# Kernel tuning notes

Hardware: AMD Instinct MI355X
Metric: run time of the kernel (lower is better)

## Reference

```python
import jax, jax.numpy as jnp
import numpy as np

N_NODES = 100000
N_EDGES = 1600000
IN_F = 128
HID = 16
NEG_SLOPE = 0.2


def setup_inputs() -> dict:
    key = jax.random.key(0)
    ks = jax.random.split(key, 12)
    x = jax.random.normal(ks[0], (N_NODES, IN_F), dtype=jnp.float32)
    edge_index = jax.random.randint(ks[1], (2, N_EDGES), 0, N_NODES, dtype=jnp.int32)
    s1 = 1.0 / np.sqrt(IN_F)
    s2 = 1.0 / np.sqrt(2 * HID)
    # layer 1: heads=2, out=16, concat -> 32
    W1 = jax.random.normal(ks[2], (IN_F, 2 * HID), dtype=jnp.float32) * s1
    a_src1 = jax.random.normal(ks[3], (2, HID), dtype=jnp.float32) * s2
    a_dst1 = jax.random.normal(ks[4], (2, HID), dtype=jnp.float32) * s2
    b1 = jnp.zeros((2 * HID,), dtype=jnp.float32)
    # layer 2: heads=1, out=1
    W2 = jax.random.normal(ks[5], (2 * HID, 1), dtype=jnp.float32) * s2
    a_src2 = jax.random.normal(ks[6], (1, 1), dtype=jnp.float32)
    a_dst2 = jax.random.normal(ks[7], (1, 1), dtype=jnp.float32)
    b2 = jnp.zeros((1,), dtype=jnp.float32)
    return {"x": x, "edge_index": edge_index, "W1": W1, "a_src1": a_src1,
            "a_dst1": a_dst1, "b1": b1, "W2": W2, "a_src2": a_src2,
            "a_dst2": a_dst2, "b2": b2}


def gat_conv(x, src, dst, W, a_src, a_dst, bias, heads, out_ch, concat):
    # PyG GATConv: linear proj, per-edge leaky-relu score, segment softmax over
    # incoming edges (dst), scatter-add aggregation. Self loops already in src/dst.
    n = x.shape[0]
    h = (x @ W).reshape(n, heads, out_ch)                      # [N,H,C]
    alpha_s = (h * a_src[None]).sum(-1)                        # [N,H]
    alpha_d = (h * a_dst[None]).sum(-1)                        # [N,H]
    e = jax.nn.leaky_relu(alpha_s[src] + alpha_d[dst], NEG_SLOPE)  # [E,H]
    m = jax.lax.stop_gradient(jax.ops.segment_max(e, dst, num_segments=n))
    ex = jnp.exp(e - m[dst])
    denom = jax.ops.segment_sum(ex, dst, num_segments=n)       # [N,H]
    alpha = ex / (denom[dst] + 1e-16)                          # [E,H]
    out = jax.ops.segment_sum(alpha[..., None] * h[src], dst, num_segments=n)  # [N,H,C]
    out = out.reshape(n, heads * out_ch) if concat else out.mean(axis=1)
    return out + bias


def reference(x, edge_index, W1, a_src1, a_dst1, b1, W2, a_src2, a_dst2, b2):
    n = x.shape[0]
    loop = jnp.arange(n, dtype=edge_index.dtype)
    src = jnp.concatenate([edge_index[0], loop])
    dst = jnp.concatenate([edge_index[1], loop])
    h = jax.nn.elu(gat_conv(x, src, dst, W1, a_src1, a_dst1, b1, 2, HID, True))
    out = gat_conv(h, src, dst, W2, a_src2, a_dst2, b2, 1, 1, False)
    return out
```

## Files before the change

kernel.cpp:

```cpp
#include <hip/hip_runtime.h>
#include <math.h>

#define IN_F 128
#define C1 32
#define NEG 0.2f
#define XPAD 132
#define BSZ 256
#define CAP 4992
#define EPB 2048

typedef _Float16 h16;
typedef _Float16 h16x2 __attribute__((ext_vector_type(2)));
typedef _Float16 h16x4 __attribute__((ext_vector_type(4)));

__device__ __forceinline__ float leaky(float x) { return x >= 0.f ? x : NEG * x; }

__global__ __launch_bounds__(256)
void k_fat(const float* __restrict__ x, const float* __restrict__ W1,
           const float* __restrict__ a_s, const float* __restrict__ a_d,
           h16* __restrict__ h1h, float* __restrict__ as1,
           float* __restrict__ ad1, int N,
           const int* __restrict__ ei, int E, int ET, int nbk,
           int* __restrict__ bcnt, int* __restrict__ ebuf, int nproj) {
    __shared__ float smem[IN_F * C1 + 32 * XPAD];
    int t = threadIdx.x;
    if ((int)blockIdx.x < nproj) {
        float* Wl = smem;
        float(*xs)[XPAD] = (float(*)[XPAD])(smem + IN_F * C1);
        for (int i = t; i < IN_F * C1 / 4; i += 256)
            ((float4*)Wl)[i] = ((const float4*)W1)[i];
        int nl = t >> 3, colq = t & 7;
        int node = blockIdx.x * 32 + nl;
        if (node < N) {
            const float4* xr = (const float4*)(x + (size_t)node * IN_F);
            #pragma unroll
            for (int q = 0; q < 4; ++q) {
                int f4 = colq + q * 8;
                *(float4*)&xs[nl][f4 * 4] = xr[f4];
            }
        }
        __syncthreads();
        if (node >= N) return;
        float4 acc = {0.f, 0.f, 0.f, 0.f};
        const float4* wp = (const float4*)Wl;
        #pragma unroll 4
        for (int k4 = 0; k4 < IN_F / 4; ++k4) {
            float4 xv = *(const float4*)&xs[nl][k4 * 4];
            float4 w0 = wp[(k4 * 4 + 0) * 8 + colq];
            float4 w1 = wp[(k4 * 4 + 1) * 8 + colq];
            float4 w2 = wp[(k4 * 4 + 2) * 8 + colq];
            float4 w3 = wp[(k4 * 4 + 3) * 8 + colq];
            acc.x = fmaf(xv.x, w0.x, acc.x); acc.y = fmaf(xv.x, w0.y, acc.y);
            acc.z = fmaf(xv.x, w0.z, acc.z); acc.w = fmaf(xv.x, w0.w, acc.w);
            acc.x = fmaf(xv.y, w1.x, acc.x); acc.y = fmaf(xv.y, w1.y, acc.y);
            acc.z = fmaf(xv.y, w1.z, acc.z); acc.w = fmaf(xv.y, w1.w, acc.w);
            acc.x = fmaf(xv.z, w2.x, acc.x); acc.y = fmaf(xv.z, w2.y, acc.y);
            acc.z = fmaf(xv.z, w2.z, acc.z); acc.w = fmaf(xv.z, w2.w, acc.w);
            acc.x = fmaf(xv.w, w3.x, acc.x); acc.y = fmaf(xv.w, w3.y, acc.y);
            acc.z = fmaf(xv.w, w3.z, acc.z); acc.w = fmaf(xv.w, w3.w, acc.w);
        }
        h16x4 hv = { (h16)acc.x, (h16)acc.y, (h16)acc.z, (h16)acc.w };
        *(h16x4*)(h1h + (size_t)node * C1 + colq * 4) = hv;
        int cb = colq * 4;
        float sv = acc.x * a_s[cb] + acc.y * a_s[cb + 1] + acc.z * a_s[cb + 2] + acc.w * a_s[cb + 3];
        float dv = acc.x * a_d[cb] + acc.y * a_d[cb + 1] + acc.z * a_d[cb + 2] + acc.w * a_d[cb + 3];
        sv += __shfl_xor(sv, 1); dv += __shfl_xor(dv, 1);
        sv += __shfl_xor(sv, 2); dv += __shfl_xor(dv, 2);
        if (colq == 0) { as1[node * 2 + 0] = sv; ad1[node * 2 + 0] = dv; }
        if (colq == 4) { as1[node * 2 + 1] = sv; ad1[node * 2 + 1] = dv; }
    } else {
        int* hist = (int*)smem;
        int* lcur = hist + 512;
        int2* ecache = (int2*)(lcur + 512);
        int bid = blockIdx.x - nproj;
        hist[t] = 0; hist[t + 256] = 0;
        __syncthreads();
        int i0 = bid * EPB, i1 = min(ET, i0 + EPB);
        for (int i = i0 + t; i < i1; i += 256) {
            int s, d;
            if (i < E) { s = ei[i]; d = ei[E + i]; } else { s = d = i - E; }
            ecache[i - i0] = make_int2(s, d);
            atomicAdd(&hist[d >> 8], 1);
        }
        __syncthreads();
        for (int b = t; b < nbk; b += 256) {
            int h = hist[b];
            int base = h ? atomicAdd(&bcnt[b], h) : 0;
            lcur[b] = b * CAP + base;
        }
        __syncthreads();
        for (int i = i0 + t; i < i1; i += 256) {
            int2 e = ecache[i - i0];
            int bkt = e.y >> 8;
            int pos = atomicAdd(&lcur[bkt], 1);
            if (pos < (bkt + 1) * CAP)
                ebuf[pos] = (e.x << 8) | (e.y & 255);
        }
    }
}

__global__ __launch_bounds__(256)
void k_bcsr(const int* __restrict__ bcnt, const int* __restrict__ ebuf,
            int N, int nbk, int ET,
            const float* __restrict__ as1, const float* __restrict__ ad1,
            int* __restrict__ off, int2* __restrict__ csr2) {
    __shared__ int deg[256];
    __shared__ int cur[256];
    __shared__ float adl[512];
    __shared__ int red[4];
    int b = blockIdx.x, t = threadIdx.x;
    int part = 0;
    for (int k = t; k < b; k += 256) part += min(bcnt[k], CAP);
    part += __shfl_xor(part, 1);  part += __shfl_xor(part, 2);
    part += __shfl_xor(part, 4);  part += __shfl_xor(part, 8);
    part += __shfl_xor(part, 16); part += __shfl_xor(part, 32);
    if ((t & 63) == 0) red[t >> 6] = part;
    int cnt = min(bcnt[b], CAP);
    int ebase = b * CAP;
    int n0 = b * BSZ;
    deg[t] = 0;
    if (n0 + t < N) ((float2*)adl)[t] = ((const float2*)ad1)[n0 + t];
    __syncthreads();
    int fbase = red[0] + red[1] + red[2] + red[3];
    if (b == nbk - 1 && t == 0) off[N] = fbase + cnt;
    for (int i = t; i < cnt; i += 256)
        atomicAdd(&deg[ebuf[ebase + i] & 255], 1);
    __syncthreads();
    int v = deg[t];
    __syncthreads();
    for (int o = 1; o < 256; o <<= 1) {
        int xv = (t >= o) ? deg[t - o] : 0; __syncthreads();
        deg[t] += xv; __syncthreads();
    }
    int excl = deg[t] - v;
    if (n0 + t < N) off[n0 + t] = fbase + excl;
    cur[t] = fbase + excl;
    __syncthreads();
    for (int i = t; i < cnt; i += 256) {
        int e = ebuf[ebase + i];
        int dl = e & 255;
        int s = e >> 8;
        float2 asv = ((const float2*)as1)[s];
        float w0 = __expf(leaky(asv.x + adl[dl * 2 + 0]));
        float w1 = __expf(leaky(asv.y + adl[dl * 2 + 1]));
        h16x2 wp = { (h16)w0, (h16)w1 };
        int p = atomicAdd(&cur[dl], 1);
        int2 rec; rec.x = s; rec.y = *(int*)&wp;
        csr2[p] = rec;
    }
}

__global__ __launch_bounds__(256)
void k_l1agg(const int* __restrict__ off, const int2* __restrict__ csr2,
             const h16* __restrict__ h1h, const float* __restrict__ b1,
             const float* __restrict__ W2, float* __restrict__ p2, int N) {
    int t = threadIdx.x;
    int node = blockIdx.x * 32 + (t >> 3);
    if (node >= N) return;
    int l = t & 7;
    int c0 = l * 4;
    int head = l >> 2;
    float den = 0.f, a0 = 0.f, a1 = 0.f, a2 = 0.f, a3 = 0.f;
    int j0 = off[node], j1 = off[node + 1];
    for (int j = j0; j < j1; j += 4) {
        #pragma unroll
        for (int k = 0; k < 4; ++k) {
            int jj = j + k;
            bool valid = jj < j1;
            jj = valid ? jj : j0;
            int2 e = csr2[jj];
            int s = e.x;
            h16x2 wv = *(h16x2*)&e.y;
            float w = valid ? (float)(head ? wv.y : wv.x) : 0.f;
            h16x4 hv = *(const h16x4*)(h1h + ((size_t)s << 5) + c0);
            den += w;
            a0 = fmaf(w, (float)hv.x, a0);
            a1 = fmaf(w, (float)hv.y, a1);
            a2 = fmaf(w, (float)hv.z, a2);
            a3 = fmaf(w, (float)hv.w, a3);
        }
    }
    float inv = 1.f / (den + 1e-16f);
    float o, val = 0.f;
    o = a0 * inv + b1[c0 + 0]; o = o > 0.f ? o : expm1f(o); val = fmaf(o, W2[c0 + 0], val);
    o = a1 * inv + b1[c0 + 1]; o = o > 0.f ? o : expm1f(o); val = fmaf(o, W2[c0 + 1], val);
    o = a2 * inv + b1[c0 + 2]; o = o > 0.f ? o : expm1f(o); val = fmaf(o, W2[c0 + 2], val);
    o = a3 * inv + b1[c0 + 3]; o = o > 0.f ? o : expm1f(o); val = fmaf(o, W2[c0 + 3], val);
    val += __shfl_xor(val, 1); val += __shfl_xor(val, 2); val += __shfl_xor(val, 4);
    if (l == 0) p2[node] = val;
}

__global__ void k_l2(const int* __restrict__ off, const int2* __restrict__ csr2,
                     const float* __restrict__ p2, const float* __restrict__ as2,
                     const float* __restrict__ ad2, const float* __restrict__ b2,
                     float* __restrict__ out, int N) {
    int i = blockIdx.x * blockDim.x + threadIdx.x;
    if (i >= N) return;
    float A = as2[0];
    float Bc = ad2[0] * p2[i];
    float den = 0.f, num = 0.f;
    int j0 = off[i], j1 = off[i + 1];
    for (int j = j0; j < j1; j += 4) {
        #pragma unroll
        for (int k = 0; k < 4; ++k) {
            int jj = j + k;
            bool valid = jj < j1;
            int s = csr2[valid ? jj : j0].x;
            float ps = p2[s];
            float w = valid ? __expf(leaky(fmaf(ps, A, Bc))) : 0.f;
            den += w;
            num = fmaf(w, ps, num);
        }
    }
    out[i] = num / (den + 1e-16f) + b2[0];
}

extern "C" void kernel_launch(void* const* d_in, const int* in_sizes, int n_in,
                              void* d_out, int out_size, void* d_ws, size_t ws_size,
                              hipStream_t stream) {
    const float* x    = (const float*)d_in[0];
    const int*   ei   = (const int*)d_in[1];
    const float* W1   = (const float*)d_in[2];
    const float* a_s1 = (const float*)d_in[3];
    const float* a_d1 = (const float*)d_in[4];
    const float* b1   = (const float*)d_in[5];
    const float* W2   = (const float*)d_in[6];
    const float* a_s2 = (const float*)d_in[7];
    const float* a_d2 = (const float*)d_in[8];
    const float* b2   = (const float*)d_in[9];
    float* out = (float*)d_out;

    const int N  = in_sizes[0] / IN_F;
    const int E  = in_sizes[1] / 2;
    const int ET = E + N;
    const int nbk = (N + BSZ - 1) / BSZ;

    float* w   = (float*)d_ws;
    float* as1 = w; w += (size_t)2 * N;
    float* ad1 = w; w += (size_t)2 * N;
    float* p2  = w; w += (size_t)N;
    h16* h1h   = (h16*)w;
    w += (size_t)16 * N;
    int* iw     = (int*)w;
    int* bcnt   = iw; iw += 512;
    int* off    = iw; iw += (N + 1);
    iw += (iw - (int*)d_ws) & 1;
    int2* csr2  = (int2*)iw; iw += (size_t)2 * ET;
    int* ebuf   = iw; iw += (size_t)nbk * CAP;

    const int B = 256;
    const int nproj = (N + 31) / 32;
    const int nblkA = (ET + EPB - 1) / EPB;

    hipMemsetAsync(bcnt, 0, 512 * sizeof(int), stream);
    k_fat  <<<nproj + nblkA, B, 0, stream>>>(x, W1, a_s1, a_d1, h1h, as1, ad1, N,
                                             ei, E, ET, nbk, bcnt, ebuf, nproj);
    k_bcsr <<<nbk, B, 0, stream>>>(bcnt, ebuf, N, nbk, ET, as1, ad1, off, csr2);
    k_l1agg<<<(N + 31) / 32, B, 0, stream>>>(off, csr2, h1h, b1, W2, p2, N);
    k_l2   <<<(N + B - 1) / B, B, 0, stream>>>(off, csr2, p2, a_s2, a_d2, b2, out, N);
}
```

Baseline: 211.8 us.

## Compute 128 nodes per projection block, batch edge loads, split layer-2 across lanes

The projection path now handles four nodes per thread group, 128 nodes per block. It reads x straight from global memory instead of staging it in shared memory, so each W1 value loaded from LDS is reused across four rows and LDS use shrinks. The CSR fill loop issues four ebuf/as1 gathers before using any of them, to expose more memory-level parallelism. Layer-2 aggregation now splits each node's edges over four lanes with shuffle reductions, which improves load balance. The trade-off is uncoalesced direct x reads, since each lane reads a different row, and possible register pressure.

```diff
diff --git a/kernel.cpp b/kernel.cpp
--- a/kernel.cpp
+++ b/kernel.cpp
@@ -4,7 +4,6 @@
 #define IN_F 128
 #define C1 32
 #define NEG 0.2f
-#define XPAD 132
 #define BSZ 256
 #define CAP 4992
 #define EPB 2048
@@ -22,54 +21,65 @@
            float* __restrict__ ad1, int N,
            const int* __restrict__ ei, int E, int ET, int nbk,
            int* __restrict__ bcnt, int* __restrict__ ebuf, int nproj) {
-    __shared__ float smem[IN_F * C1 + 32 * XPAD];
+    __shared__ int smem[5120];
     int t = threadIdx.x;
     if ((int)blockIdx.x < nproj) {
-        float* Wl = smem;
-        float(*xs)[XPAD] = (float(*)[XPAD])(smem + IN_F * C1);
+        float* Wl = (float*)smem;
         for (int i = t; i < IN_F * C1 / 4; i += 256)
             ((float4*)Wl)[i] = ((const float4*)W1)[i];
-        int nl = t >> 3, colq = t & 7;
-        int node = blockIdx.x * 32 + nl;
-        if (node < N) {
-            const float4* xr = (const float4*)(x + (size_t)node * IN_F);
-            #pragma unroll
-            for (int q = 0; q < 4; ++q) {
-                int f4 = colq + q * 8;
-                *(float4*)&xs[nl][f4 * 4] = xr[f4];
-            }
-        }
-        __syncthreads();
-        if (node >= N) return;
-        float4 acc = {0.f, 0.f, 0.f, 0.f};
+        __syncthreads();
+        int colq = t & 7, g = t >> 3;
+        int base = blockIdx.x * 128;
         const float4* wp = (const float4*)Wl;
-        #pragma unroll 4
+        int nn[4]; const float4* xp[4];
+        #pragma unroll
+        for (int j = 0; j < 4; ++j) {
+            int node = base + g + 32 * j;
+            nn[j] = node;
+            int cl = node < N ? node : 0;
+            xp[j] = (const float4*)(x + (size_t)cl * IN_F);
+        }
+        float4 acc[4];
+        #pragma unroll
+        for (int j = 0; j < 4; ++j) acc[j] = make_float4(0.f, 0.f, 0.f, 0.f);
+        #pragma unroll 2
         for (int k4 = 0; k4 < IN_F / 4; ++k4) {
-            float4 xv = *(const float4*)&xs[nl][k4 * 4];
             float4 w0 = wp[(k4 * 4 + 0) * 8 + colq];
             float4 w1 = wp[(k4 * 4 + 1) * 8 + colq];
             float4 w2 = wp[(k4 * 4 + 2) * 8 + colq];
             float4 w3 = wp[(k4 * 4 + 3) * 8 + colq];
-            acc.x = fmaf(xv.x, w0.x, acc.x); acc.y = fmaf(xv.x, w0.y, acc.y);
-            acc.z = fmaf(xv.x, w0.z, acc.z); acc.w = fmaf(xv.x, w0.w, acc.w);
-            acc.x = fmaf(xv.y, w1.x, acc.x); acc.y = fmaf(xv.y, w1.y, acc.y);
-            acc.z = fmaf(xv.y, w1.z, acc.z); acc.w = fmaf(xv.y, w1.w, acc.w);
-            acc.x = fmaf(xv.z, w2.x, acc.x); acc.y = fmaf(xv.z, w2.y, acc.y);
-            acc.z = fmaf(xv.z, w2.z, acc.z); acc.w = fmaf(xv.z, w2.w, acc.w);
-            acc.x = fmaf(xv.w, w3.x, acc.x); acc.y = fmaf(xv.w, w3.y, acc.y);
-            acc.z = fmaf(xv.w, w3.z, acc.z); acc.w = fmaf(xv.w, w3.w, acc.w);
-        }
-        h16x4 hv = { (h16)acc.x, (h16)acc.y, (h16)acc.z, (h16)acc.w };
-        *(h16x4*)(h1h + (size_t)node * C1 + colq * 4) = hv;
+            #pragma unroll
+            for (int j = 0; j < 4; ++j) {
+                float4 xv = xp[j][k4];
+                acc[j].x = fmaf(xv.x, w0.x, acc[j].x); acc[j].y = fmaf(xv.x, w0.y, acc[j].y);
+                acc[j].z = fmaf(xv.x, w0.z, acc[j].z); acc[j].w = fmaf(xv.x, w0.w, acc[j].w);
+                acc[j].x = fmaf(xv.y, w1.x, acc[j].x); acc[j].y = fmaf(xv.y, w1.y, acc[j].y);
+                acc[j].z = fmaf(xv.y, w1.z, acc[j].z); acc[j].w = fmaf(xv.y, w1.w, acc[j].w);
+                acc[j].x = fmaf(xv.z, w2.x, acc[j].x); acc[j].y = fmaf(xv.z, w2.y, acc[j].y);
+                acc[j].z = fmaf(xv.z, w2.z, acc[j].z); acc[j].w = fmaf(xv.z, w2.w, acc[j].w);
+                acc[j].x = fmaf(xv.w, w3.x, acc[j].x); acc[j].y = fmaf(xv.w, w3.y, acc[j].y);
+                acc[j].z = fmaf(xv.w, w3.z, acc[j].z); acc[j].w = fmaf(xv.w, w3.w, acc[j].w);
+            }
+        }
         int cb = colq * 4;
-        float sv = acc.x * a_s[cb] + acc.y * a_s[cb + 1] + acc.z * a_s[cb + 2] + acc.w * a_s[cb + 3];
-        float dv = acc.x * a_d[cb] + acc.y * a_d[cb + 1] + acc.z * a_d[cb + 2] + acc.w * a_d[cb + 3];
-        sv += __shfl_xor(sv, 1); dv += __shfl_xor(dv, 1);
-        sv += __shfl_xor(sv, 2); dv += __shfl_xor(dv, 2);
-        if (colq == 0) { as1[node * 2 + 0] = sv; ad1[node * 2 + 0] = dv; }
-        if (colq == 4) { as1[node * 2 + 1] = sv; ad1[node * 2 + 1] = dv; }
+        float as0 = a_s[cb], as1c = a_s[cb + 1], as2c = a_s[cb + 2], as3 = a_s[cb + 3];
+        float ad0 = a_d[cb], ad1c = a_d[cb + 1], ad2c = a_d[cb + 2], ad3 = a_d[cb + 3];
+        #pragma unroll
+        for (int j = 0; j < 4; ++j) {
+            bool vld = nn[j] < N;
+            if (vld) {
+                h16x4 hv = { (h16)acc[j].x, (h16)acc[j].y, (h16)acc[j].z, (h16)acc[j].w };
+                *(h16x4*)(h1h + (size_t)nn[j] * C1 + cb) = hv;
+            }
+            float sv = acc[j].x * as0 + acc[j].y * as1c + acc[j].z * as2c + acc[j].w * as3;
+            float dv = acc[j].x * ad0 + acc[j].y * ad1c + acc[j].z * ad2c + acc[j].w * ad3;
+            sv += __shfl_xor(sv, 1); dv += __shfl_xor(dv, 1);
+            sv += __shfl_xor(sv, 2); dv += __shfl_xor(dv, 2);
+            if (vld && colq == 0) { as1[nn[j] * 2 + 0] = sv; ad1[nn[j] * 2 + 0] = dv; }
+            if (vld && colq == 4) { as1[nn[j] * 2 + 1] = sv; ad1[nn[j] * 2 + 1] = dv; }
+        }
     } else {
-        int* hist = (int*)smem;
+        int* hist = smem;
         int* lcur = hist + 512;
         int2* ecache = (int2*)(lcur + 512);
         int bid = blockIdx.x - nproj;
@@ -136,17 +146,28 @@
     if (n0 + t < N) off[n0 + t] = fbase + excl;
     cur[t] = fbase + excl;
     __syncthreads();
-    for (int i = t; i < cnt; i += 256) {
-        int e = ebuf[ebase + i];
-        int dl = e & 255;
-        int s = e >> 8;
-        float2 asv = ((const float2*)as1)[s];
-        float w0 = __expf(leaky(asv.x + adl[dl * 2 + 0]));
-        float w1 = __expf(leaky(asv.y + adl[dl * 2 + 1]));
-        h16x2 wp = { (h16)w0, (h16)w1 };
-        int p = atomicAdd(&cur[dl], 1);
-        int2 rec; rec.x = s; rec.y = *(int*)&wp;
-        csr2[p] = rec;
+    const float2* as1v = (const float2*)as1;
+    for (int i = t; i < cnt; i += 1024) {
+        int e4[4]; float2 a4[4];
+        #pragma unroll
+        for (int k = 0; k < 4; ++k) {
+            int idx = i + k * 256;
+            bool vd = idx < cnt;
+            int e = ebuf[ebase + (vd ? idx : 0)];
+            e4[k] = vd ? e : -1;
+            a4[k] = as1v[e >> 8];
+        }
+        #pragma unroll
+        for (int k = 0; k < 4; ++k) {
+            if (e4[k] < 0) continue;
+            int dl = e4[k] & 255, s = e4[k] >> 8;
+            float w0 = __expf(leaky(a4[k].x + adl[dl * 2 + 0]));
+            float w1 = __expf(leaky(a4[k].y + adl[dl * 2 + 1]));
+            h16x2 wpk = { (h16)w0, (h16)w1 };
+            int p = atomicAdd(&cur[dl], 1);
+            int2 rec; rec.x = s; rec.y = *(int*)&wpk;
+            csr2[p] = rec;
+        }
     }
 }
 
@@ -190,29 +211,33 @@
     if (l == 0) p2[node] = val;
 }
 
-__global__ void k_l2(const int* __restrict__ off, const int2* __restrict__ csr2,
-                     const float* __restrict__ p2, const float* __restrict__ as2,
-                     const float* __restrict__ ad2, const float* __restrict__ b2,
-                     float* __restrict__ out, int N) {
-    int i = blockIdx.x * blockDim.x + threadIdx.x;
-    if (i >= N) return;
+__global__ __launch_bounds__(256)
+void k_l2(const int* __restrict__ off, const int2* __restrict__ csr2,
+          const float* __restrict__ p2, const float* __restrict__ as2,
+          const float* __restrict__ ad2, const float* __restrict__ b2,
+          float* __restrict__ out, int N) {
+    int t = threadIdx.x;
+    int node = blockIdx.x * 64 + (t >> 2);
+    if (node >= N) return;
+    int l = t & 3;
     float A = as2[0];
-    float Bc = ad2[0] * p2[i];
+    float Bc = ad2[0] * p2[node];
     float den = 0.f, num = 0.f;
-    int j0 = off[i], j1 = off[i + 1];
-    for (int j = j0; j < j1; j += 4) {
-        #pragma unroll
-        for (int k = 0; k < 4; ++k) {
-            int jj = j + k;
-            bool valid = jj < j1;
-            int s = csr2[valid ? jj : j0].x;
-            float ps = p2[s];
-            float w = valid ? __expf(leaky(fmaf(ps, A, Bc))) : 0.f;
-            den += w;
-            num = fmaf(w, ps, num);
-        }
-    }
-    out[i] = num / (den + 1e-16f) + b2[0];
+    int j0 = off[node], j1 = off[node + 1];
+    for (int j = j0 + l; j < j1; j += 8) {
+        int s0 = csr2[j].x;
+        int jb = j + 4;
+        bool vb = jb < j1;
+        int s1 = csr2[vb ? jb : j].x;
+        float ps0 = p2[s0], ps1 = p2[s1];
+        float w0 = __expf(leaky(fmaf(ps0, A, Bc)));
+        float w1 = vb ? __expf(leaky(fmaf(ps1, A, Bc))) : 0.f;
+        den += w0 + w1;
+        num = fmaf(w0, ps0, fmaf(w1, ps1, num));
+    }
+    den += __shfl_xor(den, 1); den += __shfl_xor(den, 2);
+    num += __shfl_xor(num, 1); num += __shfl_xor(num, 2);
+    if (l == 0) out[node] = num / (den + 1e-16f) + b2[0];
 }
 
 extern "C" void kernel_launch(void* const* d_in, const int* in_sizes, int n_in,
@@ -249,7 +274,7 @@
     int* ebuf   = iw; iw += (size_t)nbk * CAP;
 
     const int B = 256;
-    const int nproj = (N + 31) / 32;
+    const int nproj = (N + 127) / 128;
     const int nblkA = (ET + EPB - 1) / EPB;
 
     hipMemsetAsync(bcnt, 0, 512 * sizeof(int), stream);
@@ -257,5 +282,5 @@
                                              ei, E, ET, nbk, bcnt, ebuf, nproj);
     k_bcsr <<<nbk, B, 0, stream>>>(bcnt, ebuf, N, nbk, ET, as1, ad1, off, csr2);
     k_l1agg<<<(N + 31) / 32, B, 0, stream>>>(off, csr2, h1h, b1, W2, p2, N);
-    k_l2   <<<(N + B - 1) / B, B, 0, stream>>>(off, csr2, p2, a_s2, a_d2, b2, out, N);
-}
+    k_l2   <<<(N + 63) / 64, B, 0, stream>>>(off, csr2, p2, a_s2, a_d2, b2, out, N);
+}
```

Result: slower. 221.4 us (+4.5%).

## Aggregate both GAT layers directly from destination buckets with shared-memory atomics

Applied to the files above, without the earlier changes.

Removes the CSR build kernel and the per-node offset array. Both layers now aggregate straight from the bucketed edge buffer, one block per 128-node bucket, accumulating numerators and denominators in LDS with float atomics. Bucket size halves to 128 nodes, so the histogram and cursor arrays in the edge-binning path grow. The aim is to cut the extra global pass that wrote and reread the CSR records. The cost is heavy LDS atomic traffic, fewer and larger blocks, and edge order that is no longer deterministic.

```diff
diff --git a/kernel.cpp b/kernel.cpp
--- a/kernel.cpp
+++ b/kernel.cpp
@@ -5,12 +5,11 @@
 #define C1 32
 #define NEG 0.2f
 #define XPAD 132
-#define BSZ 256
-#define CAP 4992
+#define BSZ 128
+#define CAP 2560
 #define EPB 2048
 
 typedef _Float16 h16;
-typedef _Float16 h16x2 __attribute__((ext_vector_type(2)));
 typedef _Float16 h16x4 __attribute__((ext_vector_type(4)));
 
 __device__ __forceinline__ float leaky(float x) { return x >= 0.f ? x : NEG * x; }
@@ -70,17 +69,17 @@
         if (colq == 4) { as1[node * 2 + 1] = sv; ad1[node * 2 + 1] = dv; }
     } else {
         int* hist = (int*)smem;
-        int* lcur = hist + 512;
-        int2* ecache = (int2*)(lcur + 512);
+        int* lcur = hist + 1024;
+        int2* ecache = (int2*)(lcur + 1024);
         int bid = blockIdx.x - nproj;
-        hist[t] = 0; hist[t + 256] = 0;
+        hist[t] = 0; hist[t + 256] = 0; hist[t + 512] = 0; hist[t + 768] = 0;
         __syncthreads();
         int i0 = bid * EPB, i1 = min(ET, i0 + EPB);
         for (int i = i0 + t; i < i1; i += 256) {
             int s, d;
             if (i < E) { s = ei[i]; d = ei[E + i]; } else { s = d = i - E; }
             ecache[i - i0] = make_int2(s, d);
-            atomicAdd(&hist[d >> 8], 1);
+            atomicAdd(&hist[d >> 7], 1);
         }
         __syncthreads();
         for (int b = t; b < nbk; b += 256) {
@@ -91,128 +90,95 @@
         __syncthreads();
         for (int i = i0 + t; i < i1; i += 256) {
             int2 e = ecache[i - i0];
-            int bkt = e.y >> 8;
+            int bkt = e.y >> 7;
             int pos = atomicAdd(&lcur[bkt], 1);
             if (pos < (bkt + 1) * CAP)
-                ebuf[pos] = (e.x << 8) | (e.y & 255);
-        }
-    }
-}
-
-__global__ __launch_bounds__(256)
-void k_bcsr(const int* __restrict__ bcnt, const int* __restrict__ ebuf,
-            int N, int nbk, int ET,
-            const float* __restrict__ as1, const float* __restrict__ ad1,
-            int* __restrict__ off, int2* __restrict__ csr2) {
-    __shared__ int deg[256];
-    __shared__ int cur[256];
-    __shared__ float adl[512];
-    __shared__ int red[4];
+                ebuf[pos] = (e.x << 7) | (e.y & 127);
+        }
+    }
+}
+
+__global__ __launch_bounds__(512)
+void k_agg1(const int* __restrict__ bcnt, const int* __restrict__ ebuf,
+            int N, const float* __restrict__ as1, const float* __restrict__ ad1,
+            const float* __restrict__ b1, const float* __restrict__ W2,
+            const h16* __restrict__ h1h, float* __restrict__ p2) {
+    __shared__ float acc[BSZ][33];
+    __shared__ float den[BSZ * 3];
+    __shared__ float adl[BSZ * 2];
     int b = blockIdx.x, t = threadIdx.x;
-    int part = 0;
-    for (int k = t; k < b; k += 256) part += min(bcnt[k], CAP);
-    part += __shfl_xor(part, 1);  part += __shfl_xor(part, 2);
-    part += __shfl_xor(part, 4);  part += __shfl_xor(part, 8);
-    part += __shfl_xor(part, 16); part += __shfl_xor(part, 32);
-    if ((t & 63) == 0) red[t >> 6] = part;
     int cnt = min(bcnt[b], CAP);
     int ebase = b * CAP;
-    int n0 = b * BSZ;
-    deg[t] = 0;
-    if (n0 + t < N) ((float2*)adl)[t] = ((const float2*)ad1)[n0 + t];
-    __syncthreads();
-    int fbase = red[0] + red[1] + red[2] + red[3];
-    if (b == nbk - 1 && t == 0) off[N] = fbase + cnt;
-    for (int i = t; i < cnt; i += 256)
-        atomicAdd(&deg[ebuf[ebase + i] & 255], 1);
-    __syncthreads();
-    int v = deg[t];
-    __syncthreads();
-    for (int o = 1; o < 256; o <<= 1) {
-        int xv = (t >= o) ? deg[t - o] : 0; __syncthreads();
-        deg[t] += xv; __syncthreads();
-    }
-    int excl = deg[t] - v;
-    if (n0 + t < N) off[n0 + t] = fbase + excl;
-    cur[t] = fbase + excl;
-    __syncthreads();
-    for (int i = t; i < cnt; i += 256) {
+    int n0 = b << 7;
+    for (int i = t; i < BSZ * 33; i += 512) ((float*)acc)[i] = 0.f;
+    for (int i = t; i < BSZ * 3; i += 512) den[i] = 0.f;
+    if (t < BSZ) {
+        int n = n0 + t;
+        float2 v = (n < N) ? ((const float2*)ad1)[n] : make_float2(0.f, 0.f);
+        adl[t * 2] = v.x; adl[t * 2 + 1] = v.y;
+    }
+    __syncthreads();
+    int slot = t >> 3, l = t & 7, c0 = l * 4;
+    for (int i = slot; i < cnt; i += 64) {
         int e = ebuf[ebase + i];
-        int dl = e & 255;
-        int s = e >> 8;
+        int dl = e & 127, s = e >> 7;
         float2 asv = ((const float2*)as1)[s];
         float w0 = __expf(leaky(asv.x + adl[dl * 2 + 0]));
         float w1 = __expf(leaky(asv.y + adl[dl * 2 + 1]));
-        h16x2 wp = { (h16)w0, (h16)w1 };
-        int p = atomicAdd(&cur[dl], 1);
-        int2 rec; rec.x = s; rec.y = *(int*)&wp;
-        csr2[p] = rec;
-    }
-}
-
-__global__ __launch_bounds__(256)
-void k_l1agg(const int* __restrict__ off, const int2* __restrict__ csr2,
-             const h16* __restrict__ h1h, const float* __restrict__ b1,
-             const float* __restrict__ W2, float* __restrict__ p2, int N) {
-    int t = threadIdx.x;
-    int node = blockIdx.x * 32 + (t >> 3);
-    if (node >= N) return;
-    int l = t & 7;
-    int c0 = l * 4;
-    int head = l >> 2;
-    float den = 0.f, a0 = 0.f, a1 = 0.f, a2 = 0.f, a3 = 0.f;
-    int j0 = off[node], j1 = off[node + 1];
-    for (int j = j0; j < j1; j += 4) {
-        #pragma unroll
-        for (int k = 0; k < 4; ++k) {
-            int jj = j + k;
-            bool valid = jj < j1;
-            jj = valid ? jj : j0;
-            int2 e = csr2[jj];
-            int s = e.x;
-            h16x2 wv = *(h16x2*)&e.y;
-            float w = valid ? (float)(head ? wv.y : wv.x) : 0.f;
-            h16x4 hv = *(const h16x4*)(h1h + ((size_t)s << 5) + c0);
-            den += w;
-            a0 = fmaf(w, (float)hv.x, a0);
-            a1 = fmaf(w, (float)hv.y, a1);
-            a2 = fmaf(w, (float)hv.z, a2);
-            a3 = fmaf(w, (float)hv.w, a3);
-        }
-    }
-    float inv = 1.f / (den + 1e-16f);
-    float o, val = 0.f;
-    o = a0 * inv + b1[c0 + 0]; o = o > 0.f ? o : expm1f(o); val = fmaf(o, W2[c0 + 0], val);
-    o = a1 * inv + b1[c0 + 1]; o = o > 0.f ? o : expm1f(o); val = fmaf(o, W2[c0 + 1], val);
-    o = a2 * inv + b1[c0 + 2]; o = o > 0.f ? o : expm1f(o); val = fmaf(o, W2[c0 + 2], val);
-    o = a3 * inv + b1[c0 + 3]; o = o > 0.f ? o : expm1f(o); val = fmaf(o, W2[c0 + 3], val);
-    val += __shfl_xor(val, 1); val += __shfl_xor(val, 2); val += __shfl_xor(val, 4);
-    if (l == 0) p2[node] = val;
-}
-
-__global__ void k_l2(const int* __restrict__ off, const int2* __restrict__ csr2,
-                     const float* __restrict__ p2, const float* __restrict__ as2,
-                     const float* __restrict__ ad2, const float* __restrict__ b2,
-                     float* __restrict__ out, int N) {
-    int i = blockIdx.x * blockDim.x + threadIdx.x;
-    if (i >= N) return;
-    float A = as2[0];
-    float Bc = ad2[0] * p2[i];
-    float den = 0.f, num = 0.f;
-    int j0 = off[i], j1 = off[i + 1];
-    for (int j = j0; j < j1; j += 4) {
-        #pragma unroll
-        for (int k = 0; k < 4; ++k) {
-            int jj = j + k;
-            bool valid = jj < j1;
-            int s = csr2[valid ? jj : j0].x;
-            float ps = p2[s];
-            float w = valid ? __expf(leaky(fmaf(ps, A, Bc))) : 0.f;
-            den += w;
-            num = fmaf(w, ps, num);
-        }
-    }
-    out[i] = num / (den + 1e-16f) + b2[0];
+        float wh = (c0 < 16) ? w0 : w1;
+        h16x4 hv = *(const h16x4*)(h1h + ((size_t)s << 5) + c0);
+        atomicAdd(&acc[dl][c0 + 0], wh * (float)hv.x);
+        atomicAdd(&acc[dl][c0 + 1], wh * (float)hv.y);
+        atomicAdd(&acc[dl][c0 + 2], wh * (float)hv.z);
+        atomicAdd(&acc[dl][c0 + 3], wh * (float)hv.w);
+        if (l == 0) atomicAdd(&den[dl * 3 + 0], w0);
+        if (l == 4) atomicAdd(&den[dl * 3 + 1], w1);
+    }
+    __syncthreads();
+    int head = c0 >> 4;
+    float b1l[4] = { b1[c0], b1[c0 + 1], b1[c0 + 2], b1[c0 + 3] };
+    float w2l[4] = { W2[c0], W2[c0 + 1], W2[c0 + 2], W2[c0 + 3] };
+    #pragma unroll
+    for (int p = 0; p < 2; ++p) {
+        int dl = slot + p * 64;
+        int node = n0 + dl;
+        float inv = 1.f / (den[dl * 3 + head] + 1e-16f);
+        float val = 0.f, o;
+        o = acc[dl][c0 + 0] * inv + b1l[0]; o = o > 0.f ? o : expm1f(o); val = fmaf(o, w2l[0], val);
+        o = acc[dl][c0 + 1] * inv + b1l[1]; o = o > 0.f ? o : expm1f(o); val = fmaf(o, w2l[1], val);
+        o = acc[dl][c0 + 2] * inv + b1l[2]; o = o > 0.f ? o : expm1f(o); val = fmaf(o, w2l[2], val);
+        o = acc[dl][c0 + 3] * inv + b1l[3]; o = o > 0.f ? o : expm1f(o); val = fmaf(o, w2l[3], val);
+        val += __shfl_xor(val, 1); val += __shfl_xor(val, 2); val += __shfl_xor(val, 4);
+        if (l == 0 && node < N) p2[node] = val;
+    }
+}
+
+__global__ __launch_bounds__(512)
+void k_agg2(const int* __restrict__ bcnt, const int* __restrict__ ebuf,
+            int N, const float* __restrict__ p2, const float* __restrict__ as2,
+            const float* __restrict__ ad2, const float* __restrict__ b2,
+            float* __restrict__ out) {
+    __shared__ float nd[BSZ * 3];
+    __shared__ float p2l[BSZ];
+    int b = blockIdx.x, t = threadIdx.x;
+    int cnt = min(bcnt[b], CAP);
+    int ebase = b * CAP;
+    int n0 = b << 7;
+    for (int i = t; i < BSZ * 3; i += 512) nd[i] = 0.f;
+    if (t < BSZ) { int n = n0 + t; p2l[t] = (n < N) ? p2[n] : 0.f; }
+    __syncthreads();
+    float A = as2[0], Ad = ad2[0];
+    for (int i = t; i < cnt; i += 512) {
+        int e = ebuf[ebase + i];
+        int dl = e & 127, s = e >> 7;
+        float ps = p2[s];
+        float w = __expf(leaky(fmaf(ps, A, Ad * p2l[dl])));
+        atomicAdd(&nd[dl * 3 + 0], w);
+        atomicAdd(&nd[dl * 3 + 1], w * ps);
+    }
+    __syncthreads();
+    if (t < BSZ && n0 + t < N)
+        out[n0 + t] = nd[t * 3 + 1] / (nd[t * 3 + 0] + 1e-16f) + b2[0];
 }
 
 extern "C" void kernel_launch(void* const* d_in, const int* in_sizes, int n_in,
@@ -242,20 +208,16 @@
     h16* h1h   = (h16*)w;
     w += (size_t)16 * N;
     int* iw     = (int*)w;
-    int* bcnt   = iw; iw += 512;
-    int* off    = iw; iw += (N + 1);
-    iw += (iw - (int*)d_ws) & 1;
-    int2* csr2  = (int2*)iw; iw += (size_t)2 * ET;
+    int* bcnt   = iw; iw += 1024;
     int* ebuf   = iw; iw += (size_t)nbk * CAP;
 
     const int B = 256;
     const int nproj = (N + 31) / 32;
     const int nblkA = (ET + EPB - 1) / EPB;
 
-    hipMemsetAsync(bcnt, 0, 512 * sizeof(int), stream);
-    k_fat  <<<nproj + nblkA, B, 0, stream>>>(x, W1, a_s1, a_d1, h1h, as1, ad1, N,
-                                             ei, E, ET, nbk, bcnt, ebuf, nproj);
-    k_bcsr <<<nbk, B, 0, stream>>>(bcnt, ebuf, N, nbk, ET, as1, ad1, off, csr2);
-    k_l1agg<<<(N + 31) / 32, B, 0, stream>>>(off, csr2, h1h, b1, W2, p2, N);
-    k_l2   <<<(N + B - 1) / B, B, 0, stream>>>(off, csr2, p2, a_s2, a_d2, b2, out, N);
-}
+    hipMemsetAsync(bcnt, 0, 1024 * sizeof(int), stream);
+    k_fat <<<nproj + nblkA, B, 0, stream>>>(x, W1, a_s1, a_d1, h1h, as1, ad1, N,
+                                            ei, E, ET, nbk, bcnt, ebuf, nproj);
+    k_agg1<<<nbk, 512, 0, stream>>>(bcnt, ebuf, N, as1, ad1, b1, W2, h1h, p2);
+    k_agg2<<<nbk, 512, 0, stream>>>(bcnt, ebuf, N, p2, a_s2, a_d2, b2, out);
+}
```

New measurement: 551.0 us. 160% more time.

## Compute layer-1 projection with MFMA f16 tiles instead of scalar FMAs

Applied to the files above, without the earlier changes.

Replaces the LDS-staged scalar fp32 FMA projection x@W1 with a 16x16x32 f16 MFMA path. Each wave keeps W1 fragments in registers, loads x rows straight from global, and computes two 16-column tiles for TPW node tiles. The attention dot products are reduced with 16-lane shuffles. This removes the LDS staging and the block-wide sync, and shrinks the shared-memory footprint. The cost is inputs rounded to fp16 before the matmul, which lowers precision, and per-element h16 stores that are less vectorised.

```diff
diff --git a/kernel.cpp b/kernel.cpp
--- a/kernel.cpp
+++ b/kernel.cpp
@@ -4,14 +4,16 @@
 #define IN_F 128
 #define C1 32
 #define NEG 0.2f
-#define XPAD 132
 #define BSZ 256
 #define CAP 4992
 #define EPB 2048
+#define TPW 2
 
 typedef _Float16 h16;
 typedef _Float16 h16x2 __attribute__((ext_vector_type(2)));
 typedef _Float16 h16x4 __attribute__((ext_vector_type(4)));
+typedef _Float16 h16x8 __attribute__((ext_vector_type(8)));
+typedef float f32x4 __attribute__((ext_vector_type(4)));
 
 __device__ __forceinline__ float leaky(float x) { return x >= 0.f ? x : NEG * x; }
 
@@ -22,54 +24,63 @@
            float* __restrict__ ad1, int N,
            const int* __restrict__ ei, int E, int ET, int nbk,
            int* __restrict__ bcnt, int* __restrict__ ebuf, int nproj) {
-    __shared__ float smem[IN_F * C1 + 32 * XPAD];
+    __shared__ int smem[5120];
     int t = threadIdx.x;
     if ((int)blockIdx.x < nproj) {
-        float* Wl = smem;
-        float(*xs)[XPAD] = (float(*)[XPAD])(smem + IN_F * C1);
-        for (int i = t; i < IN_F * C1 / 4; i += 256)
-            ((float4*)Wl)[i] = ((const float4*)W1)[i];
-        int nl = t >> 3, colq = t & 7;
-        int node = blockIdx.x * 32 + nl;
-        if (node < N) {
-            const float4* xr = (const float4*)(x + (size_t)node * IN_F);
+        int wid = t >> 6, lane = t & 63;
+        int q = lane >> 4, r = lane & 15;
+        h16x8 Bf[2][4];
+        #pragma unroll
+        for (int ct = 0; ct < 2; ++ct)
             #pragma unroll
-            for (int q = 0; q < 4; ++q) {
-                int f4 = colq + q * 8;
-                *(float4*)&xs[nl][f4 * 4] = xr[f4];
+            for (int kc = 0; kc < 4; ++kc)
+                #pragma unroll
+                for (int j = 0; j < 8; ++j)
+                    Bf[ct][kc][j] = (h16)W1[(kc * 32 + q * 8 + j) * C1 + ct * 16 + r];
+        float a_s0 = a_s[r], a_s1v = a_s[16 + r];
+        float a_d0 = a_d[r], a_d1v = a_d[16 + r];
+        #pragma unroll
+        for (int tt = 0; tt < TPW; ++tt) {
+            int tile = (blockIdx.x * 4 + wid) * TPW + tt;
+            int m0 = tile << 4;
+            if (m0 >= N) break;
+            int row = m0 + r; if (row >= N) row = N - 1;
+            const float* xr = x + (size_t)row * IN_F + q * 8;
+            f32x4 acc0 = {0.f, 0.f, 0.f, 0.f};
+            f32x4 acc1 = {0.f, 0.f, 0.f, 0.f};
+            #pragma unroll
+            for (int kc = 0; kc < 4; ++kc) {
+                float4 xa = *(const float4*)(xr + kc * 32);
+                float4 xb = *(const float4*)(xr + kc * 32 + 4);
+                h16x8 A;
+                A[0] = (h16)xa.x; A[1] = (h16)xa.y; A[2] = (h16)xa.z; A[3] = (h16)xa.w;
+                A[4] = (h16)xb.x; A[5] = (h16)xb.y; A[6] = (h16)xb.z; A[7] = (h16)xb.w;
+                acc0 = __builtin_amdgcn_mfma_f32_16x16x32_f16(A, Bf[0][kc], acc0, 0, 0, 0);
+                acc1 = __builtin_amdgcn_mfma_f32_16x16x32_f16(A, Bf[1][kc], acc1, 0, 0, 0);
             }
-        }
-        __syncthreads();
-        if (node >= N) return;
-        float4 acc = {0.f, 0.f, 0.f, 0.f};
-        const float4* wp = (const float4*)Wl;
-        #pragma unroll 4
-        for (int k4 = 0; k4 < IN_F / 4; ++k4) {
-            float4 xv = *(const float4*)&xs[nl][k4 * 4];
-            float4 w0 = wp[(k4 * 4 + 0) * 8 + colq];
-            float4 w1 = wp[(k4 * 4 + 1) * 8 + colq];
-            float4 w2 = wp[(k4 * 4 + 2) * 8 + colq];
-            float4 w3 = wp[(k4 * 4 + 3) * 8 + colq];
-            acc.x = fmaf(xv.x, w0.x, acc.x); acc.y = fmaf(xv.x, w0.y, acc.y);
-            acc.z = fmaf(xv.x, w0.z, acc.z); acc.w = fmaf(xv.x, w0.w, acc.w);
-            acc.x = fmaf(xv.y, w1.x, acc.x); acc.y = fmaf(xv.y, w1.y, acc.y);
-            acc.z = fmaf(xv.y, w1.z, acc.z); acc.w = fmaf(xv.y, w1.w, acc.w);
-            acc.x = fmaf(xv.z, w2.x, acc.x); acc.y = fmaf(xv.z, w2.y, acc.y);
-            acc.z = fmaf(xv.z, w2.z, acc.z); acc.w = fmaf(xv.z, w2.w, acc.w);
-            acc.x = fmaf(xv.w, w3.x, acc.x); acc.y = fmaf(xv.w, w3.y, acc.y);
-            acc.z = fmaf(xv.w, w3.z, acc.z); acc.w = fmaf(xv.w, w3.w, acc.w);
-        }
-        h16x4 hv = { (h16)acc.x, (h16)acc.y, (h16)acc.z, (h16)acc.w };
-        *(h16x4*)(h1h + (size_t)node * C1 + colq * 4) = hv;
-        int cb = colq * 4;
-        float sv = acc.x * a_s[cb] + acc.y * a_s[cb + 1] + acc.z * a_s[cb + 2] + acc.w * a_s[cb + 3];
-        float dv = acc.x * a_d[cb] + acc.y * a_d[cb + 1] + acc.z * a_d[cb + 2] + acc.w * a_d[cb + 3];
-        sv += __shfl_xor(sv, 1); dv += __shfl_xor(dv, 1);
-        sv += __shfl_xor(sv, 2); dv += __shfl_xor(dv, 2);
-        if (colq == 0) { as1[node * 2 + 0] = sv; ad1[node * 2 + 0] = dv; }
-        if (colq == 4) { as1[node * 2 + 1] = sv; ad1[node * 2 + 1] = dv; }
+            #pragma unroll
+            for (int reg = 0; reg < 4; ++reg) {
+                int node = m0 + q * 4 + reg;
+                bool vld = node < N;
+                float h0 = acc0[reg], h1 = acc1[reg];
+                if (vld) {
+                    h1h[(size_t)node * C1 + r]      = (h16)h0;
+                    h1h[(size_t)node * C1 + 16 + r] = (h16)h1;
+                }
+                float s0 = h0 * a_s0, s1 = h1 * a_s1v;
+                float d0 = h0 * a_d0, d1 = h1 * a_d1v;
+                s0 += __shfl_xor(s0, 1); s0 += __shfl_xor(s0, 2); s0 += __shfl_xor(s0, 4); s0 += __shfl_xor(s0, 8);
+                s1 += __shfl_xor(s1, 1); s1 += __shfl_xor(s1, 2); s1 += __shfl_xor(s1, 4); s1 += __shfl_xor(s1, 8);
+                d0 += __shfl_xor(d0, 1); d0 += __shfl_xor(d0, 2); d0 += __shfl_xor(d0, 4); d0 += __shfl_xor(d0, 8);
+                d1 += __shfl_xor(d1, 1); d1 += __shfl_xor(d1, 2); d1 += __shfl_xor(d1, 4); d1 += __shfl_xor(d1, 8);
+                if (vld && r == 0) {
+                    *(float2*)&as1[node * 2] = make_float2(s0, s1);
+                    *(float2*)&ad1[node * 2] = make_float2(d0, d1);
+                }
+            }
+        }
     } else {
-        int* hist = (int*)smem;
+        int* hist = smem;
         int* lcur = hist + 512;
         int2* ecache = (int2*)(lcur + 512);
         int bid = blockIdx.x - nproj;
@@ -249,7 +260,8 @@
     int* ebuf   = iw; iw += (size_t)nbk * CAP;
 
     const int B = 256;
-    const int nproj = (N + 31) / 32;
+    const int ntile = (N + 15) / 16;
+    const int nproj = (ntile + 4 * TPW - 1) / (4 * TPW);
     const int nblkA = (ET + EPB - 1) / EPB;
 
     hipMemsetAsync(bcnt, 0, 512 * sizeof(int), stream);
```

Measured after the change: 199.9 us. 5.7% less time.
